# Kernel optimization log

Hardware: AMD Instinct MI355X
Metric: run time of the kernel (lower is better)

The kernel has to match this reference:

```python
import math
import jax, jax.numpy as jnp
import numpy as np

EMBED_DIM = 1024
NUM_HEADS = 16
HEAD_DIM = EMBED_DIM // NUM_HEADS
NUM_BUCKETS = 32
MAX_DISTANCE = 128


def _relative_position_bucket(relative_position, num_buckets=NUM_BUCKETS, max_distance=MAX_DISTANCE):
    # Bidirectional T5 bucketing (matches torch reference exactly).
    num_buckets = num_buckets // 2
    relative_buckets = (relative_position > 0).astype(jnp.int32) * num_buckets
    relative_position = jnp.abs(relative_position)
    max_exact = num_buckets // 2
    is_small = relative_position < max_exact
    rp_large = jnp.log(relative_position.astype(jnp.float32) / max_exact) / math.log(max_distance / max_exact)
    rp_large = max_exact + (rp_large * (num_buckets - max_exact)).astype(jnp.int32)
    rp_large = jnp.minimum(rp_large, num_buckets - 1)
    relative_buckets = relative_buckets + jnp.where(is_small, relative_position, rp_large)
    return relative_buckets


def compute_bias(rel_emb, query_length, key_length):
    context_position = jnp.arange(query_length, dtype=jnp.int32)[:, None]
    memory_position = jnp.arange(key_length, dtype=jnp.int32)[None, :]
    relative_position = memory_position - context_position  # [q, k]
    buckets = _relative_position_bucket(relative_position)
    values = rel_emb[buckets]                 # [q, k, h]
    return jnp.transpose(values, (2, 0, 1))[None]  # [1, h, q, k]


def setup_inputs() -> dict:
    key = jax.random.key(0)
    k1, k2, k3, k4 = jax.random.split(key, 4)
    B, S = 2, 2048
    hidden_states = jax.random.normal(k1, (B, S, EMBED_DIM), dtype=jnp.float32)
    scale = 1.0 / math.sqrt(EMBED_DIM)
    W_qkv = jax.random.normal(k2, (EMBED_DIM, 3 * EMBED_DIM), dtype=jnp.float32) * scale
    W_out = jax.random.normal(k3, (EMBED_DIM, EMBED_DIM), dtype=jnp.float32) * scale
    rel_emb = jax.random.normal(k4, (NUM_BUCKETS, NUM_HEADS), dtype=jnp.float32) * 0.02
    return {"hidden_states": hidden_states, "W_qkv": W_qkv, "W_out": W_out, "rel_emb": rel_emb}


def reference(hidden_states, W_qkv, W_out, rel_emb):
    B, S, _ = hidden_states.shape
    qkv = hidden_states @ W_qkv                                # [B, S, 3*D]
    qkv = qkv.reshape(B, S, 3, NUM_HEADS, HEAD_DIM)
    qkv = jnp.transpose(qkv, (0, 3, 2, 1, 4))                  # [B, H, 3, S, dh]
    q, k, v = qkv[:, :, 0], qkv[:, :, 1], qkv[:, :, 2]
    scores = jnp.einsum('bhqd,bhkd->bhqk', q, k)               # no 1/sqrt(d) scaling (T5 style)
    scores = scores + compute_bias(rel_emb, S, S)
    attn = jax.nn.softmax(scores.astype(jnp.float32), axis=-1).astype(scores.dtype)
    out = jnp.einsum('bhqk,bhkd->bhqd', attn, v)               # [B, H, S, dh]
    out = jnp.transpose(out, (0, 2, 1, 3)).reshape(B, S, EMBED_DIM)
    return out @ W_out
```

## Files before the change

kernel.cpp:

```cpp
#include <hip/hip_runtime.h>
#include <hip/hip_bf16.h>
#include <math.h>

typedef _Float16 f16;
typedef __attribute__((ext_vector_type(8))) _Float16 f16x8;
typedef __attribute__((ext_vector_type(4))) _Float16 f16x4;
typedef __attribute__((ext_vector_type(2))) _Float16 f16x2;
typedef __attribute__((ext_vector_type(4))) float f32x4;

#define EMBED 1024
#define NHEADS 16
#define HDIM 64
#define BATCH 2
#define SEQ 2048
#define BS 4096
#define LOG2E 1.4426950408889634f


__device__ __forceinline__ f32x4 mfma16x32(f16x8 a, f16x8 b, f32x4 c) {
  return __builtin_amdgcn_mfma_f32_16x16x32_f16(a, b, c, 0, 0, 0);
}
__device__ __forceinline__ f32x4 mfma16x16(f16x4 a, f16x4 b, f32x4 c) {
  return __builtin_amdgcn_mfma_f32_16x16x16f16(a, b, c, 0, 0, 0);
}
__device__ __forceinline__ f16x2 cvt_pk(float a, float b) {
  return __builtin_bit_cast(f16x2, __builtin_amdgcn_cvt_pkrtz(a, b));
}
__device__ __forceinline__ void gload_lds16(const f16* __restrict__ g, f16* l) {
  __builtin_amdgcn_global_load_lds(
      (const __attribute__((address_space(1))) void*)g,
      (__attribute__((address_space(3))) void*)l, 16, 0, 0);
}

__global__ void prep_kernel(const float* __restrict__ X, const float* __restrict__ Wqkv,
                            const float* __restrict__ Wout, const float* __restrict__ rel_emb,
                            f16* __restrict__ Xh, f16* __restrict__ Wqkv_t,
                            f16* __restrict__ Wout_t, float* __restrict__ btab) {
  __shared__ float tile[32][33];
  int bid = blockIdx.x, tid = threadIdx.x;
  if (bid < 4096) {
    int i = (bid * 256 + tid) * 4;
    float4 v = *(const float4*)(X + i);
    f16x4 o = { (f16)v.x, (f16)v.y, (f16)v.z, (f16)v.w };
    *(f16x4*)(Xh + i) = o;
  } else if (bid < 8192) {
    const float* in;
    f16* out;
    int N, idx;
    if (bid < 7168) { in = Wqkv; out = Wqkv_t; N = 3072; idx = bid - 4096; }
    else            { in = Wout; out = Wout_t; N = 1024; idx = bid - 7168; }
    int nt = N / 32;
    int n0 = (idx % nt) * 32, k0 = (idx / nt) * 32;
    int tx = tid & 31, ty = tid >> 5;
#pragma unroll
    for (int r = ty; r < 32; r += 8) tile[r][tx] = in[(size_t)(k0 + r) * N + n0 + tx];
    __syncthreads();
#pragma unroll
    for (int r = ty; r < 32; r += 8) out[(size_t)(n0 + r) * 1024 + k0 + tx] = (f16)tile[tx][r];
  } else {
    int idx = (bid - 8192) * 256 + tid;
    if (idx >= 4095) return;
    int rp = idx - 2047;
    int rb = rp > 0 ? 16 : 0;
    int arp = rp < 0 ? -rp : rp;
    int loc;
    if (arp < 8) {
      loc = arp;
    } else {
      float lr = logf((float)arp * 0.125f) * (1.0f / 2.7725887222397811f);
      int t = 8 + (int)(lr * 8.0f);
      loc = t < 15 ? t : 15;
    }
    int bucket = rb + loc;
#pragma unroll
    for (int h = 0; h < 16; h++) btab[h * 4095 + idx] = rel_emb[bucket * 16 + h] * LOG2E;
  }
}

__device__ __forceinline__ void gemm_core(const f16* __restrict__ A, const f16* __restrict__ Bt,
                                          int m0, int n0, int Kdim, f32x4 (&acc)[4][4]) {
  __shared__ __align__(16) f16 As[128 * 32];
  __shared__ __align__(16) f16 Bs[128 * 32];

  int tid = threadIdx.x;
  int lane = tid & 63, wave = tid >> 6;
  int l15 = lane & 15, quad = lane >> 4;
  int wr = (wave >> 1) * 64, wc = (wave & 1) * 64;
  int rowl = lane >> 2;
  int col8 = (lane & 3) * 8;

#pragma unroll
  for (int i = 0; i < 4; i++)
#pragma unroll
    for (int j = 0; j < 4; j++) acc[i][j] = f32x4{0.f, 0.f, 0.f, 0.f};

  for (int kt = 0; kt < Kdim / 32; kt++) {
    int kk = kt * 32;
#pragma unroll
    for (int c = 0; c < 2; c++) {
      int row = wave * 32 + c * 16 + rowl;
      gload_lds16(A + (size_t)(m0 + row) * Kdim + kk + col8, &As[(wave * 32 + c * 16) * 32]);
      gload_lds16(Bt + (size_t)(n0 + row) * Kdim + kk + col8, &Bs[(wave * 32 + c * 16) * 32]);
    }
    __syncthreads();
    f16x8 af[4], bf[4];
#pragma unroll
    for (int i = 0; i < 4; i++) af[i] = *(const f16x8*)(&As[(wr + i * 16 + l15) * 32 + quad * 8]);
#pragma unroll
    for (int j = 0; j < 4; j++) bf[j] = *(const f16x8*)(&Bs[(wc + j * 16 + l15) * 32 + quad * 8]);
#pragma unroll
    for (int i = 0; i < 4; i++)
#pragma unroll
      for (int j = 0; j < 4; j++) acc[i][j] = mfma16x32(af[i], bf[j], acc[i][j]);
    __syncthreads();
  }
}

__global__ __launch_bounds__(256, 3) void gemm_qkv_kernel(
    const f16* __restrict__ Xh, const f16* __restrict__ Wt,
    f16* __restrict__ Q, f16* __restrict__ K_, f16* __restrict__ Vp) {
  f32x4 acc[4][4];
  int m0 = blockIdx.y * 128, n0 = blockIdx.x * 128;
  gemm_core(Xh, Wt, m0, n0, 1024, acc);

  int lane = threadIdx.x & 63, wave = threadIdx.x >> 6;
  int l15 = lane & 15, quad = lane >> 4;
  int wr = (wave >> 1) * 64, wc = (wave & 1) * 64;
  int nq = n0 + wc;
  int which = nq >> 10;
  int h = (nq >> 6) & 15;
  int b = m0 >> 11;

  if (which == 2) {
    int s0 = (m0 & 2047) + wr;
    f16* vbase = Vp + (size_t)(b * 16 + h) * 131072 + (size_t)(s0 >> 6) * 4096;
#pragma unroll
    for (int i = 0; i < 4; i++) {
#pragma unroll
      for (int jp = 0; jp < 2; jp++) {
        f16x8 pk = { (f16)acc[i][2 * jp][0],     (f16)acc[i][2 * jp][1],
                     (f16)acc[i][2 * jp][2],     (f16)acc[i][2 * jp][3],
                     (f16)acc[i][2 * jp + 1][0], (f16)acc[i][2 * jp + 1][1],
                     (f16)acc[i][2 * jp + 1][2], (f16)acc[i][2 * jp + 1][3] };
        *(f16x8*)(vbase + (i * 2 + jp) * 512 + lane * 8) = pk;
      }
    }
  } else {
    f16* base = (which == 0) ? Q : K_;
    float sc = (which == 0) ? LOG2E : 1.0f;
#pragma unroll
    for (int i = 0; i < 4; i++) {
#pragma unroll
      for (int j = 0; j < 4; j++) {
        int d = j * 16 + l15;
#pragma unroll
        for (int r = 0; r < 4; r++) {
          int m = m0 + wr + i * 16 + quad * 4 + r;
          int s = m & 2047;
          base[(((size_t)(b * 16 + h) * 2048 + s) << 6) + d] = (f16)(acc[i][j][r] * sc);
        }
      }
    }
  }
}

__global__ void repack_k_kernel(const f16* __restrict__ Kw, f16* __restrict__ Kp) {
  int o = blockIdx.x * 256 + threadIdx.x;
  int lane = o & 63;
  int ct = (o >> 6) & 7;
  int kt = (o >> 9) & 31;
  int bh = o >> 14;
  int c = ct >> 1, t = ct & 1;
  int l15 = lane & 15, quad = lane >> 4;
  int s = kt * 64 + c * 16 + l15;
  f16x8 v = *(const f16x8*)(Kw + ((size_t)(bh * 2048 + s) << 6) + t * 32 + quad * 8);
  *(f16x8*)(Kp + (size_t)o * 8) = v;
}

__global__ __launch_bounds__(256, 4) void attn_kernel(
    const f16* __restrict__ Q, const f16* __restrict__ Kp, const f16* __restrict__ Vp,
    const float* __restrict__ btab, f16* __restrict__ O) {
  __shared__ float bias_lds[2112];

  int qt = blockIdx.x, bh = blockIdx.y;
  int qbase = qt * 64;
  int h = bh & 15, b = bh >> 4;
  int tid = threadIdx.x, lane = tid & 63, wave = tid >> 6;
  int l15 = lane & 15, quad = lane >> 4;

  const float* brow = btab + h * 4095 + (1984 - qbase);
  for (int i = tid; i < 2111; i += 256) bias_lds[i] = brow[i];

  const f16* qptr = Q + ((size_t)bh * 2048 + qbase + wave * 16 + l15) * 64 + quad * 8;
  f16x8 qf0 = *(const f16x8*)(qptr);
  f16x8 qf1 = *(const f16x8*)(qptr + 32);

  f32x4 accO[4] = {};
  float m_i = -INFINITY, l_i = 0.f;

  const f16* kc = Kp + (size_t)bh * 131072 + 1792;
  const f16* vc = Vp + (size_t)bh * 131072 + 1792;
  const int voff = lane * 8;
  const int bofs = quad * 4 - wave * 16 - l15 + 63;

  __syncthreads();

  for (int kt = 0; kt < 32; kt++) {
    const float* bb = &bias_lds[kt * 64 + bofs];
    f32x4 scT[4];
#pragma unroll
    for (int c = 0; c < 4; c++) {
      scT[c] = f32x4{ bb[c * 16], bb[c * 16 + 1], bb[c * 16 + 2], bb[c * 16 + 3] };
      f16x8 kf0 = *(const f16x8*)(kc + ((c * 2 + 0) * 512 - 1792) + voff);
      f16x8 kf1 = *(const f16x8*)(kc + ((c * 2 + 1) * 512 - 1792) + voff);
      scT[c] = mfma16x32(kf0, qf0, scT[c]);
      scT[c] = mfma16x32(kf1, qf1, scT[c]);
    }
    f16x8 vf8[4][2];
#pragma unroll
    for (int c = 0; c < 4; c++)
#pragma unroll
      for (int jp = 0; jp < 2; jp++)
        vf8[c][jp] = *(const f16x8*)(vc + ((c * 2 + jp) * 512 - 1792) + voff);
    float mp0 = fmaxf(fmaxf(scT[0][0], scT[0][1]), fmaxf(scT[0][2], scT[0][3]));
    float mp1 = fmaxf(fmaxf(scT[1][0], scT[1][1]), fmaxf(scT[1][2], scT[1][3]));
    float mp2 = fmaxf(fmaxf(scT[2][0], scT[2][1]), fmaxf(scT[2][2], scT[2][3]));
    float mp3 = fmaxf(fmaxf(scT[3][0], scT[3][1]), fmaxf(scT[3][2], scT[3][3]));
    float mp = fmaxf(fmaxf(mp0, mp1), fmaxf(mp2, mp3));
    if (__any(mp > m_i)) {
      float mx = fmaxf(mp, __shfl_xor(mp, 16));
      mx = fmaxf(mx, __shfl_xor(mx, 32));
      float mn = fmaxf(m_i, mx);
      float alpha = exp2f(m_i - mn);
      m_i = mn;
      l_i *= alpha;
      float arow[4];
#pragma unroll
      for (int r = 0; r < 4; r++) arow[r] = __shfl(alpha, quad * 4 + r);
#pragma unroll
      for (int d = 0; d < 4; d++)
#pragma unroll
        for (int r = 0; r < 4; r++) accO[d][r] *= arow[r];
    }
    float mx = m_i;
    f16x4 p[4];
    float rc[4];
#pragma unroll
    for (int c = 0; c < 4; c++) {
      float e0 = exp2f(scT[c][0] - mx);
      float e1 = exp2f(scT[c][1] - mx);
      float e2 = exp2f(scT[c][2] - mx);
      float e3 = exp2f(scT[c][3] - mx);
      rc[c] = (e0 + e1) + (e2 + e3);
      f16x2 plo = cvt_pk(e0, e1);
      f16x2 phi = cvt_pk(e2, e3);
      p[c][0] = plo[0]; p[c][1] = plo[1]; p[c][2] = phi[0]; p[c][3] = phi[1];
    }
    float rs = (rc[0] + rc[1]) + (rc[2] + rc[3]);
    rs += __shfl_xor(rs, 16);
    rs += __shfl_xor(rs, 32);
    l_i += rs;
#pragma unroll
    for (int c = 0; c < 4; c++) {
#pragma unroll
      for (int jp = 0; jp < 2; jp++) {
        f16x4 vlo = __builtin_shufflevector(vf8[c][jp], vf8[c][jp], 0, 1, 2, 3);
        f16x4 vhi = __builtin_shufflevector(vf8[c][jp], vf8[c][jp], 4, 5, 6, 7);
        accO[2 * jp]     = mfma16x16(p[c], vlo, accO[2 * jp]);
        accO[2 * jp + 1] = mfma16x16(p[c], vhi, accO[2 * jp + 1]);
      }
    }
    kc += 4096;
    vc += 4096;
  }

  float linv = 1.0f / l_i;
  float lrow[4];
#pragma unroll
  for (int r = 0; r < 4; r++) lrow[r] = __shfl(linv, quad * 4 + r);
#pragma unroll
  for (int dblk = 0; dblk < 4; dblk++) {
#pragma unroll
    for (int r = 0; r < 4; r++) {
      int q = qbase + wave * 16 + quad * 4 + r;
      O[((size_t)(b * 2048 + q) << 10) + h * 64 + dblk * 16 + l15] = (f16)(accO[dblk][r] * lrow[r]);
    }
  }
}

__global__ __launch_bounds__(256, 2) void gemm_out_kernel(
    const f16* __restrict__ Oh, const f16* __restrict__ Wt, float* __restrict__ out) {
  __shared__ __align__(16) f16 As[128 * 32];
  __shared__ __align__(16) f16 Bs[64 * 32];

  int tid = threadIdx.x;
  int lane = tid & 63, wave = tid >> 6;
  int l15 = lane & 15, quad = lane >> 4;
  int rowl = lane >> 2;
  int col8 = (lane & 3) * 8;
  int m0 = blockIdx.y * 128, n0 = blockIdx.x * 64;
  int wr = wave * 32;

  f32x4 acc[2][4];
#pragma unroll
  for (int i = 0; i < 2; i++)
#pragma unroll
    for (int j = 0; j < 4; j++) acc[i][j] = f32x4{0.f, 0.f, 0.f, 0.f};

  for (int kt = 0; kt < 32; kt++) {
    int kk = kt * 32;
#pragma unroll
    for (int c = 0; c < 2; c++) {
      int row = wave * 32 + c * 16 + rowl;
      gload_lds16(Oh + (size_t)(m0 + row) * 1024 + kk + col8, &As[(wave * 32 + c * 16) * 32]);
    }
    {
      int row = wave * 16 + rowl;
      gload_lds16(Wt + (size_t)(n0 + row) * 1024 + kk + col8, &Bs[(wave * 16) * 32]);
    }
    __syncthreads();
    f16x8 af[2], bf[4];
#pragma unroll
    for (int i = 0; i < 2; i++) af[i] = *(const f16x8*)(&As[(wr + i * 16 + l15) * 32 + quad * 8]);
#pragma unroll
    for (int j = 0; j < 4; j++) bf[j] = *(const f16x8*)(&Bs[(j * 16 + l15) * 32 + quad * 8]);
#pragma unroll
    for (int i = 0; i < 2; i++)
#pragma unroll
      for (int j = 0; j < 4; j++) acc[i][j] = mfma16x32(af[i], bf[j], acc[i][j]);
    __syncthreads();
  }

#pragma unroll
  for (int i = 0; i < 2; i++) {
#pragma unroll
    for (int j = 0; j < 4; j++) {
      int n = n0 + j * 16 + l15;
#pragma unroll
      for (int r = 0; r < 4; r++) {
        int m = m0 + wr + i * 16 + quad * 4 + r;
        out[((size_t)m << 10) + n] = acc[i][j][r];
      }
    }
  }
}

extern "C" void kernel_launch(void* const* d_in, const int* in_sizes, int n_in,
                              void* d_out, int out_size, void* d_ws, size_t ws_size,
                              hipStream_t stream) {
  const float* X = (const float*)d_in[0];
  const float* Wqkv = (const float*)d_in[1];
  const float* Wout = (const float*)d_in[2];
  const float* rel = (const float*)d_in[3];

  char* ws = (char*)d_ws;
  f16* Xh     = (f16*)(ws + 0);
  f16* Kp     = (f16*)(ws + 0);
  f16* Wqkv_t = (f16*)(ws + 8388608);
  f16* Wout_t = (f16*)(ws + 14680064);
  f16* Qw     = (f16*)(ws + 16777216);
  f16* Kw     = (f16*)(ws + 25165824);
  f16* Vp     = (f16*)(ws + 33554432);
  f16* Ow     = (f16*)(ws + 41943040);
  float* btab = (float*)(ws + 50331648);

  prep_kernel<<<8208, 256, 0, stream>>>(X, Wqkv, Wout, rel, Xh, Wqkv_t, Wout_t, btab);
  gemm_qkv_kernel<<<dim3(24, 32), 256, 0, stream>>>(Xh, Wqkv_t, Qw, Kw, Vp);
  repack_k_kernel<<<2048, 256, 0, stream>>>(Kw, Kp);
  attn_kernel<<<dim3(32, 32), 256, 0, stream>>>(Qw, Kp, Vp, btab, Ow);
  gemm_out_kernel<<<dim3(16, 32), 256, 0, stream>>>(Ow, Wout_t, (float*)d_out);
}
```

Baseline: 224.9 us.

## Use 16x16x32 MFMA for PV by permuting K/V layouts, defer row-sum reduction

The K repack and V store layouts are permuted so the P fragments from the QK^T MFMA line up with the K dimension of a 16x16x32 MFMA. The PV product then runs as 8 wider MFMAs per tile instead of 16 16x16x16 ones, and the bias load offsets change to match. The per-tile cross-lane row-sum shuffles are replaced by a per-lane accumulator that is reduced once at the end. It also switches to hardware exp2 and rcp intrinsics, which lowers instruction count but may slightly change numerics.

New measurement: 213.8 us. -4.9%, faster.

```diff
diff --git a/kernel.cpp b/kernel.cpp
--- a/kernel.cpp
+++ b/kernel.cpp
@@ -19,9 +19,6 @@
 
 __device__ __forceinline__ f32x4 mfma16x32(f16x8 a, f16x8 b, f32x4 c) {
   return __builtin_amdgcn_mfma_f32_16x16x32_f16(a, b, c, 0, 0, 0);
-}
-__device__ __forceinline__ f32x4 mfma16x16(f16x4 a, f16x4 b, f32x4 c) {
-  return __builtin_amdgcn_mfma_f32_16x16x16f16(a, b, c, 0, 0, 0);
 }
 __device__ __forceinline__ f16x2 cvt_pk(float a, float b) {
   return __builtin_bit_cast(f16x2, __builtin_amdgcn_cvt_pkrtz(a, b));
@@ -134,15 +131,16 @@
   if (which == 2) {
     int s0 = (m0 & 2047) + wr;
     f16* vbase = Vp + (size_t)(b * 16 + h) * 131072 + (size_t)(s0 >> 6) * 4096;
+    int qr_lo = (quad >> 1);
+    int joff = (quad & 1) * 4;
 #pragma unroll
     for (int i = 0; i < 4; i++) {
-#pragma unroll
-      for (int jp = 0; jp < 2; jp++) {
-        f16x8 pk = { (f16)acc[i][2 * jp][0],     (f16)acc[i][2 * jp][1],
-                     (f16)acc[i][2 * jp][2],     (f16)acc[i][2 * jp][3],
-                     (f16)acc[i][2 * jp + 1][0], (f16)acc[i][2 * jp + 1][1],
-                     (f16)acc[i][2 * jp + 1][2], (f16)acc[i][2 * jp + 1][3] };
-        *(f16x8*)(vbase + (i * 2 + jp) * 512 + lane * 8) = pk;
+      int cc = i >> 1;
+      int qr = (i & 1) * 2 + qr_lo;
+#pragma unroll
+      for (int j = 0; j < 4; j++) {
+        f16x4 pk = { (f16)acc[i][j][0], (f16)acc[i][j][1], (f16)acc[i][j][2], (f16)acc[i][j][3] };
+        *(f16x4*)(vbase + (cc * 4 + j) * 512 + (qr * 16 + l15) * 8 + joff) = pk;
       }
     }
   } else {
@@ -171,8 +169,9 @@
   int kt = (o >> 9) & 31;
   int bh = o >> 14;
   int c = ct >> 1, t = ct & 1;
-  int l15 = lane & 15, quad = lane >> 4;
-  int s = kt * 64 + c * 16 + l15;
+  int cc = c >> 1, g = c & 1;
+  int l15 = lane & 15, quad = lane >> 4;
+  int s = kt * 64 + cc * 32 + ((l15 >> 2) << 3) + (g << 2) + (l15 & 3);
   f16x8 v = *(const f16x8*)(Kw + ((size_t)(bh * 2048 + s) << 6) + t * 32 + quad * 8);
   *(f16x8*)(Kp + (size_t)o * 8) = v;
 }
@@ -196,44 +195,48 @@
   f16x8 qf1 = *(const f16x8*)(qptr + 32);
 
   f32x4 accO[4] = {};
-  float m_i = -INFINITY, l_i = 0.f;
+  float m_i = -INFINITY;
+  float l_acc = 0.f;
 
   const f16* kc = Kp + (size_t)bh * 131072 + 1792;
   const f16* vc = Vp + (size_t)bh * 131072 + 1792;
   const int voff = lane * 8;
-  const int bofs = quad * 4 - wave * 16 - l15 + 63;
+  const int bofs = quad * 8 - wave * 16 - l15 + 63;
 
   __syncthreads();
 
   for (int kt = 0; kt < 32; kt++) {
     const float* bb = &bias_lds[kt * 64 + bofs];
     f32x4 scT[4];
+    scT[0] = f32x4{ bb[0],  bb[1],  bb[2],  bb[3]  };
+    scT[1] = f32x4{ bb[4],  bb[5],  bb[6],  bb[7]  };
+    scT[2] = f32x4{ bb[32], bb[33], bb[34], bb[35] };
+    scT[3] = f32x4{ bb[36], bb[37], bb[38], bb[39] };
 #pragma unroll
     for (int c = 0; c < 4; c++) {
-      scT[c] = f32x4{ bb[c * 16], bb[c * 16 + 1], bb[c * 16 + 2], bb[c * 16 + 3] };
       f16x8 kf0 = *(const f16x8*)(kc + ((c * 2 + 0) * 512 - 1792) + voff);
       f16x8 kf1 = *(const f16x8*)(kc + ((c * 2 + 1) * 512 - 1792) + voff);
       scT[c] = mfma16x32(kf0, qf0, scT[c]);
       scT[c] = mfma16x32(kf1, qf1, scT[c]);
     }
-    f16x8 vf8[4][2];
-#pragma unroll
-    for (int c = 0; c < 4; c++)
-#pragma unroll
-      for (int jp = 0; jp < 2; jp++)
-        vf8[c][jp] = *(const f16x8*)(vc + ((c * 2 + jp) * 512 - 1792) + voff);
-    float mp0 = fmaxf(fmaxf(scT[0][0], scT[0][1]), fmaxf(scT[0][2], scT[0][3]));
-    float mp1 = fmaxf(fmaxf(scT[1][0], scT[1][1]), fmaxf(scT[1][2], scT[1][3]));
-    float mp2 = fmaxf(fmaxf(scT[2][0], scT[2][1]), fmaxf(scT[2][2], scT[2][3]));
-    float mp3 = fmaxf(fmaxf(scT[3][0], scT[3][1]), fmaxf(scT[3][2], scT[3][3]));
-    float mp = fmaxf(fmaxf(mp0, mp1), fmaxf(mp2, mp3));
+    f16x8 vf[2][4];
+#pragma unroll
+    for (int cc = 0; cc < 2; cc++)
+#pragma unroll
+      for (int dblk = 0; dblk < 4; dblk++)
+        vf[cc][dblk] = *(const f16x8*)(vc + ((cc * 4 + dblk) * 512 - 1792) + voff);
+    float mp0 = fmaxf(fmaxf(fmaxf(scT[0][0], scT[0][1]), scT[0][2]), scT[0][3]);
+    float mp1 = fmaxf(fmaxf(fmaxf(scT[1][0], scT[1][1]), scT[1][2]), scT[1][3]);
+    float mp2 = fmaxf(fmaxf(fmaxf(scT[2][0], scT[2][1]), scT[2][2]), scT[2][3]);
+    float mp3 = fmaxf(fmaxf(fmaxf(scT[3][0], scT[3][1]), scT[3][2]), scT[3][3]);
+    float mp = fmaxf(fmaxf(fmaxf(mp0, mp1), mp2), mp3);
     if (__any(mp > m_i)) {
       float mx = fmaxf(mp, __shfl_xor(mp, 16));
       mx = fmaxf(mx, __shfl_xor(mx, 32));
       float mn = fmaxf(m_i, mx);
-      float alpha = exp2f(m_i - mn);
+      float alpha = __builtin_amdgcn_exp2f(m_i - mn);
       m_i = mn;
-      l_i *= alpha;
+      l_acc *= alpha;
       float arow[4];
 #pragma unroll
       for (int r = 0; r < 4; r++) arow[r] = __shfl(alpha, quad * 4 + r);
@@ -244,37 +247,31 @@
     }
     float mx = m_i;
     f16x4 p[4];
-    float rc[4];
 #pragma unroll
     for (int c = 0; c < 4; c++) {
-      float e0 = exp2f(scT[c][0] - mx);
-      float e1 = exp2f(scT[c][1] - mx);
-      float e2 = exp2f(scT[c][2] - mx);
-      float e3 = exp2f(scT[c][3] - mx);
-      rc[c] = (e0 + e1) + (e2 + e3);
+      float e0 = __builtin_amdgcn_exp2f(scT[c][0] - mx);
+      float e1 = __builtin_amdgcn_exp2f(scT[c][1] - mx);
+      float e2 = __builtin_amdgcn_exp2f(scT[c][2] - mx);
+      float e3 = __builtin_amdgcn_exp2f(scT[c][3] - mx);
+      l_acc += (e0 + e1) + (e2 + e3);
       f16x2 plo = cvt_pk(e0, e1);
       f16x2 phi = cvt_pk(e2, e3);
       p[c][0] = plo[0]; p[c][1] = plo[1]; p[c][2] = phi[0]; p[c][3] = phi[1];
     }
-    float rs = (rc[0] + rc[1]) + (rc[2] + rc[3]);
-    rs += __shfl_xor(rs, 16);
-    rs += __shfl_xor(rs, 32);
-    l_i += rs;
-#pragma unroll
-    for (int c = 0; c < 4; c++) {
-#pragma unroll
-      for (int jp = 0; jp < 2; jp++) {
-        f16x4 vlo = __builtin_shufflevector(vf8[c][jp], vf8[c][jp], 0, 1, 2, 3);
-        f16x4 vhi = __builtin_shufflevector(vf8[c][jp], vf8[c][jp], 4, 5, 6, 7);
-        accO[2 * jp]     = mfma16x16(p[c], vlo, accO[2 * jp]);
-        accO[2 * jp + 1] = mfma16x16(p[c], vhi, accO[2 * jp + 1]);
-      }
-    }
+    f16x8 pp0 = __builtin_shufflevector(p[0], p[1], 0, 1, 2, 3, 4, 5, 6, 7);
+    f16x8 pp1 = __builtin_shufflevector(p[2], p[3], 0, 1, 2, 3, 4, 5, 6, 7);
+#pragma unroll
+    for (int dblk = 0; dblk < 4; dblk++) accO[dblk] = mfma16x32(pp0, vf[0][dblk], accO[dblk]);
+#pragma unroll
+    for (int dblk = 0; dblk < 4; dblk++) accO[dblk] = mfma16x32(pp1, vf[1][dblk], accO[dblk]);
     kc += 4096;
     vc += 4096;
   }
 
-  float linv = 1.0f / l_i;
+  float lt = l_acc;
+  lt += __shfl_xor(lt, 16);
+  lt += __shfl_xor(lt, 32);
+  float linv = __builtin_amdgcn_rcpf(lt);
   float lrow[4];
 #pragma unroll
   for (int r = 0; r < 4; r++) lrow[r] = __shfl(linv, quad * 4 + r);
```
